# Kernel tuning notes

Measured on AMD Instinct MI355X. Metric: run time of the kernel, lower is better.

Reference implementation:

```python
import jax, jax.numpy as jnp
import numpy as np

T, B, NIN, NOUT, H, NLAYER = 512, 32, 72, 90, 512, 5


def _ln(x, g, b):
    m = jnp.mean(x, -1, keepdims=True)
    v = jnp.var(x, -1, keepdims=True)
    return (x - m) * jax.lax.rsqrt(v + 1e-5) * g + b


def _sru_dir(xt, fp, rp, hw, vf, vr, bf, br):
    # xt/fp/rp/hw: (T, B, H) in scan order; elementwise gated recurrence
    def step(c, inp):
        x_t, f_t, r_t, hw_t = inp
        f = jax.nn.sigmoid(f_t + vf * c + bf)
        r = jax.nn.sigmoid(r_t + vr * c + br)
        c2 = f * c + (1.0 - f) * x_t
        h = r * jnp.tanh(c2) + (1.0 - r) * hw_t
        return c2, h
    c0 = jnp.zeros_like(xt[0])
    cT, hs = jax.lax.scan(step, c0, (xt, fp, rp, hw))
    return hs, cT


def _sru_layer(x, W, v, b, g, be, k):
    # x: (T, B, d_in); W: (d_in, 2*k*H); v,b: (2 dirs, 2 gates, H)
    Tl, Bl = x.shape[0], x.shape[1]
    xn = _ln(x, g, be)
    U = (xn @ W).reshape(Tl, Bl, 2, k, H)
    outs, cs = [], []
    for d in range(2):
        Ud = U[:, :, d]
        if d == 1:
            Ud = jnp.flip(Ud, 0)
        # highway: extra projection when d_in != H (k=4), else raw input (k=3)
        hw = Ud[:, :, 3] if k == 4 else (jnp.flip(x, 0) if d == 1 else x)
        hs, cT = _sru_dir(Ud[:, :, 0], Ud[:, :, 1], Ud[:, :, 2], hw,
                          v[d, 0], v[d, 1], b[d, 0], b[d, 1])
        if d == 1:
            hs = jnp.flip(hs, 0)
        outs.append(hs)
        cs.append(cT)
    return jnp.concatenate(outs, -1), jnp.concatenate(cs, -1)


def setup_inputs() -> dict:
    key = jax.random.key(0)
    ks = jax.random.split(key, 12)
    s1 = 1.0 / np.sqrt(NIN)
    s2 = 1.0 / np.sqrt(2 * H)
    s0 = 1.0 / np.sqrt(H)
    return {
        "x": jax.random.normal(ks[0], (T, B, NIN), jnp.float32),
        "W1": jax.random.normal(ks[1], (NIN, H), jnp.float32) * s1,
        "b1": jnp.zeros((H,), jnp.float32),
        "W2": jax.random.normal(ks[2], (2 * H, NOUT), jnp.float32) * s2,
        "b2": jnp.zeros((NOUT,), jnp.float32),
        # SRU layer 0: input H -> 2 dirs * H, k=3 (highway uses raw input)
        "W0": jax.random.normal(ks[3], (H, 2 * 3 * H), jnp.float32) * s0,
        "v0": jax.random.normal(ks[4], (2, 2, H), jnp.float32) * s0,
        "bb0": jnp.zeros((2, 2, H), jnp.float32),
        "g0": jnp.ones((H,), jnp.float32),
        "be0": jnp.zeros((H,), jnp.float32),
        # SRU layers 1..4: input 2H -> 2 dirs * H, k=4 (projected highway)
        "Ws": jax.random.normal(ks[5], (NLAYER - 1, 2 * H, 2 * 4 * H), jnp.float32) * s2,
        "vs": jax.random.normal(ks[6], (NLAYER - 1, 2, 2, H), jnp.float32) * s0,
        "bbs": jnp.zeros((NLAYER - 1, 2, 2, H), jnp.float32),
        "gs": jnp.ones((NLAYER - 1, 2 * H), jnp.float32),
        "bes": jnp.zeros((NLAYER - 1, 2 * H), jnp.float32),
    }


def reference(x, W1, b1, W2, b2, W0, v0, bb0, g0, be0, Ws, vs, bbs, gs, bes):
    h = jax.nn.relu(x @ W1 + b1)  # (T, B, H); dropout is identity at eval
    states = []
    h, c = _sru_layer(h, W0, v0, bb0, g0, be0, 3)
    states.append(c)
    for i in range(Ws.shape[0]):
        h, c = _sru_layer(h, Ws[i], vs[i], bbs[i], gs[i], bes[i], 4)
        states.append(c)
    out = h @ W2 + b2  # (T, B, NOUT)
    return out, jnp.stack(states)  # h state: (NLAYER, B, 2H)
```

## Files before the change

kernel.cpp:

```cpp
#include <hip/hip_runtime.h>
#include <stdint.h>

#define T_LEN 512
#define BATCH 32
#define NIN   72
#define NOUT  90
#define HDIM  512
#define MROWS (T_LEN*BATCH)

typedef unsigned short u16;
typedef unsigned int   u32;

typedef __bf16 bf16x8 __attribute__((ext_vector_type(8)));
typedef short  s16x8  __attribute__((ext_vector_type(8)));
typedef float  f32x4  __attribute__((ext_vector_type(4)));

__device__ __forceinline__ float b2f(u16 u){ return __uint_as_float(((u32)u)<<16); }
__device__ __forceinline__ u16 f2b(float x){
  u32 u = __float_as_uint(x);
  u += 0x7FFFu + ((u>>16)&1u);
  return (u16)(u>>16);
}
__device__ __forceinline__ float sigmoidf_(float z){ return 1.f/(1.f+__expf(-z)); }
__device__ __forceinline__ float tanhf_(float z){ return 2.f/(1.f+__expf(-2.f*z)) - 1.f; }

__device__ __forceinline__ void gload16(const void* g, void* l){
  __builtin_amdgcn_global_load_lds(
      (const __attribute__((address_space(1))) void*)g,
      (__attribute__((address_space(3))) void*)l, 16, 0, 0);
}

__global__ __launch_bounds__(256) void k_transpose_cast(
    const float* __restrict__ S, u16* __restrict__ D, int K, int N, int ldd)
{
  __shared__ float t[32][33];
  int k0 = blockIdx.y*32, n0 = blockIdx.x*32;
  int tx = threadIdx.x, ty = threadIdx.y;
  #pragma unroll
  for (int i=0;i<4;++i){
    int k = k0 + ty + i*8, n = n0 + tx;
    if (k < K && n < N) t[ty+i*8][tx] = S[(size_t)k*N + n];
  }
  __syncthreads();
  #pragma unroll
  for (int i=0;i<4;++i){
    int n = n0 + ty + i*8, k = k0 + tx;
    if (n < N && k < K) D[(size_t)n*ldd + k] = f2b(t[tx][ty+i*8]);
  }
}

__global__ __launch_bounds__(256) void k_gemm1_relu(
    const float* __restrict__ X, const float* __restrict__ W1,
    const float* __restrict__ b1, u16* __restrict__ H0)
{
  __shared__ float As[64][73];
  __shared__ float Bs[72][64];
  int m0 = blockIdx.y*64, n0 = blockIdx.x*64;
  int tid = threadIdx.x;
  for (int idx=tid; idx<64*NIN; idx+=256){ int r=idx/NIN, k=idx-r*NIN; As[r][k] = X[(size_t)(m0+r)*NIN + k]; }
  for (int idx=tid; idx<NIN*64; idx+=256){ int k=idx>>6, n=idx&63; Bs[k][n] = W1[(size_t)k*HDIM + n0+n]; }
  __syncthreads();
  int tx = tid & 15, ty = tid >> 4;
  float acc[4][4] = {};
  for (int k=0;k<NIN;++k){
    float a[4], bv[4];
    #pragma unroll
    for (int i=0;i<4;++i) a[i]=As[ty*4+i][k];
    #pragma unroll
    for (int j=0;j<4;++j) bv[j]=Bs[k][tx*4+j];
    #pragma unroll
    for (int i=0;i<4;++i)
      #pragma unroll
      for (int j=0;j<4;++j) acc[i][j] += a[i]*bv[j];
  }
  #pragma unroll
  for (int i=0;i<4;++i){
    int row = m0 + ty*4 + i;
    #pragma unroll
    for (int j=0;j<4;++j){
      int col = n0 + tx*4 + j;
      float v = acc[i][j] + b1[col];
      H0[(size_t)row*HDIM + col] = f2b(v > 0.f ? v : 0.f);
    }
  }
}

template<int D>
__global__ __launch_bounds__(256) void k_ln(
    const u16* __restrict__ X, const float* __restrict__ g,
    const float* __restrict__ be, u16* __restrict__ Y)
{
  int wrow = (blockIdx.x*256 + threadIdx.x) >> 6;
  int lane = threadIdx.x & 63;
  constexpr int E = D/64;
  const u16* row = X + (size_t)wrow*D;
  float vals[E];
  float s=0.f, s2=0.f;
  #pragma unroll
  for (int i=0;i<E/4;++i){
    ushort4 u = *(const ushort4*)(row + i*256 + lane*4);
    float v0=b2f(u.x), v1=b2f(u.y), v2=b2f(u.z), v3=b2f(u.w);
    vals[i*4+0]=v0; vals[i*4+1]=v1; vals[i*4+2]=v2; vals[i*4+3]=v3;
    s  += v0+v1+v2+v3;
    s2 += v0*v0+v1*v1+v2*v2+v3*v3;
  }
  #pragma unroll
  for (int off=32; off; off>>=1){ s += __shfl_xor(s,off); s2 += __shfl_xor(s2,off); }
  float mean = s * (1.f/D);
  float var  = s2 * (1.f/D) - mean*mean;
  float rstd = rsqrtf(var + 1e-5f);
  u16* yr = Y + (size_t)wrow*D;
  #pragma unroll
  for (int i=0;i<E/4;++i){
    int col = i*256 + lane*4;
    float4 gg = *(const float4*)(g+col);
    float4 bb = *(const float4*)(be+col);
    ushort4 o;
    o.x = f2b((vals[i*4+0]-mean)*rstd*gg.x + bb.x);
    o.y = f2b((vals[i*4+1]-mean)*rstd*gg.y + bb.y);
    o.z = f2b((vals[i*4+2]-mean)*rstd*gg.z + bb.z);
    o.w = f2b((vals[i*4+3]-mean)*rstd*gg.w + bb.w);
    *(ushort4*)(yr + col) = o;
  }
}

__global__ __launch_bounds__(512, 2) void k_gemm256(
    const u16* __restrict__ A, const u16* __restrict__ BT,
    u16* __restrict__ C, int K, int N)
{
  __shared__ u16 lds[65536];
  const int tid  = threadIdx.x;
  const int lane = tid & 63;
  const int wid  = tid >> 6;
  const int wm   = wid >> 2;
  const int wn   = wid & 3;

  const int nbx = gridDim.x;
  const int nwg = nbx * gridDim.y;
  const int bid = blockIdx.y * nbx + blockIdx.x;
  const int cpx = nwg >> 3;
  const int swz = (bid & 7) * cpx + (bid >> 3);
  const int m0 = (swz / nbx) * 256;
  const int n0 = (swz % nbx) * 256;

  const int l3 = lane >> 3, l7 = lane & 7;
  const int kswz = (l7 ^ l3) * 8;

  auto stageA = [&](int ts, int h, int db){
    const u16* base = A + (size_t)(m0 + h*128 + wid*8 + l3)*K + ts*64 + kswz;
    u16* dst = lds + db*32768 + h*8192 + wid*512;
    gload16(base,               dst);
    gload16(base + (size_t)64*K, dst + 4096);
  };
  auto stageB = [&](int ts, int db){
    const u16* base = BT + (size_t)(n0 + wid*8 + l3)*K + ts*64 + kswz;
    u16* dst = lds + db*32768 + 16384 + wid*512;
    gload16(base,                dst);
    gload16(base + (size_t) 64*K, dst + 4096);
    gload16(base + (size_t)128*K, dst + 8192);
    gload16(base + (size_t)192*K, dst + 12288);
  };
  auto rdfrag = [&](const u16* buf, int row, int ks)->bf16x8 {
    int byte = (row*128 + (ks*32 + ((lane>>4)*8))*2) ^ ((row&7)<<4);
    return __builtin_bit_cast(bf16x8, *(const s16x8*)((const char*)buf + byte));
  };

  f32x4 acc[8][4] = {};
  const int nt = K >> 6;

  stageB(0, 0);
  stageA(0, 0, 0);
  stageA(0, 1, 0);

  for (int t = 0; t < nt; ++t){
    const u16* bufA = lds + (t & 1)*32768;
    const u16* bufB = bufA + 16384;
    const int tn = (t+1 < nt) ? t+1 : t;
    const int db = (t+1) & 1;

    stageB(tn, db);
    stageA(tn, 0, db);
    stageA(tn, 1, db);
    asm volatile("s_waitcnt vmcnt(8)" ::: "memory");
    __builtin_amdgcn_sched_barrier(0);
    __builtin_amdgcn_s_barrier();
    __builtin_amdgcn_sched_barrier(0);

    bf16x8 bfr[4][2];
    #pragma unroll
    for (int n=0;n<4;++n)
      #pragma unroll
      for (int ks=0;ks<2;++ks)
        bfr[n][ks] = rdfrag(bufB, wn*64 + n*16 + (lane&15), ks);
    bf16x8 afr[2][2][2];
    #pragma unroll
    for (int mm=0;mm<2;++mm)
      #pragma unroll
      for (int ks=0;ks<2;++ks)
        afr[0][mm][ks] = rdfrag(bufA, wm*128 + mm*16 + (lane&15), ks);

    #pragma unroll
    for (int q=0;q<4;++q){
      asm volatile("s_waitcnt lgkmcnt(0)" ::: "memory");
      __builtin_amdgcn_sched_barrier(0);
      __builtin_amdgcn_s_setprio(1);
      #pragma unroll
      for (int mm=0;mm<2;++mm)
        #pragma unroll
        for (int n=0;n<4;++n)
          #pragma unroll
          for (int ks=0;ks<2;++ks)
            acc[q*2+mm][n] = __builtin_amdgcn_mfma_f32_16x16x32_bf16(
                afr[q&1][mm][ks], bfr[n][ks], acc[q*2+mm][n], 0,0,0);
      __builtin_amdgcn_s_setprio(0);
      if (q < 3){
        #pragma unroll
        for (int mm=0;mm<2;++mm)
          #pragma unroll
          for (int ks=0;ks<2;++ks)
            afr[(q+1)&1][mm][ks] = rdfrag(bufA, wm*128 + ((q+1)*2+mm)*16 + (lane&15), ks);
      } else {
        asm volatile("s_waitcnt lgkmcnt(0)" ::: "memory");
      }
      __builtin_amdgcn_sched_barrier(0);
      __builtin_amdgcn_s_barrier();
      __builtin_amdgcn_sched_barrier(0);
    }
  }

  #pragma unroll
  for (int m=0;m<8;++m){
    int row = m0 + wm*128 + m*16 + ((lane>>4)<<2);
    #pragma unroll
    for (int n=0;n<4;++n){
      int col = n0 + wn*64 + n*16 + (lane&15);
      #pragma unroll
      for (int i=0;i<4;++i)
        C[(size_t)(row+i)*N + col] = f2b(acc[m][n][i]);
    }
  }
}

template<bool OUT_F32, bool HAS_BIAS>
__global__ __launch_bounds__(256) void k_gemm(
    const u16* __restrict__ A, const u16* __restrict__ BT,
    void* __restrict__ Cv, const float* __restrict__ bias,
    int K, int N, int ldc, int nbound)
{
  __shared__ u16 As[128*64];
  __shared__ u16 Bs[128*64];
  const int tid  = threadIdx.x;
  const int lane = tid & 63;
  const int wid  = tid >> 6;

  const int nbx = gridDim.x;
  const int nwg = nbx * gridDim.y;
  const int bid = blockIdx.y * nbx + blockIdx.x;
  const int cpx = nwg >> 3;
  const int swzb = (bid & 7) * cpx + (bid >> 3);
  const int bx = swzb % nbx, by = swzb / nbx;

  const int m0 = by * 128;
  const int n0 = bx * 128;
  const int wr = wid >> 1, wc = wid & 1;
  f32x4 acc[4][4] = {};

  const int srow = lane >> 3;
  const int skel = (lane & 7) * 8;

  for (int kt = 0; kt < K; kt += 64) {
    #pragma unroll
    for (int i=0;i<4;++i){
      int seg  = wid*4 + i;
      int arow = seg*8 + srow;
      gload16(A  + (size_t)(m0 + arow)*K + kt + skel, As + seg*512);
      gload16(BT + (size_t)(n0 + arow)*K + kt + skel, Bs + seg*512);
    }
    __syncthreads();
    #pragma unroll
    for (int ks=0; ks<2; ++ks){
      bf16x8 a[4], b[4];
      #pragma unroll
      for (int m=0;m<4;++m){
        int off = (wr*64 + m*16 + (lane&15))*64 + ks*32 + (lane>>4)*8;
        a[m] = __builtin_bit_cast(bf16x8, *(const s16x8*)(As + off));
      }
      #pragma unroll
      for (int n=0;n<4;++n){
        int off = (wc*64 + n*16 + (lane&15))*64 + ks*32 + (lane>>4)*8;
        b[n] = __builtin_bit_cast(bf16x8, *(const s16x8*)(Bs + off));
      }
      #pragma unroll
      for (int m=0;m<4;++m)
        #pragma unroll
        for (int n=0;n<4;++n)
          acc[m][n] = __builtin_amdgcn_mfma_f32_16x16x32_bf16(a[m], b[n], acc[m][n], 0,0,0);
    }
    __syncthreads();
  }

  #pragma unroll
  for (int m=0;m<4;++m){
    #pragma unroll
    for (int n=0;n<4;++n){
      int col = n0 + wc*64 + n*16 + (lane & 15);
      #pragma unroll
      for (int i=0;i<4;++i){
        int row = m0 + wr*64 + m*16 + ((lane>>4)<<2) + i;
        float v = acc[m][n][i];
        if (OUT_F32) {
          if (col < nbound){
            float bv = HAS_BIAS ? bias[col] : 0.f;
            ((float*)Cv)[(size_t)row*ldc + col] = v + bv;
          }
        } else {
          ((u16*)Cv)[(size_t)row*ldc + col] = f2b(v);
        }
      }
    }
  }
}

template<int KG>
__global__ __launch_bounds__(64) void k_scan(
    const u16* __restrict__ U, const u16* __restrict__ hwsrc,
    const float* __restrict__ v, const float* __restrict__ bb,
    u16* __restrict__ hout, float* __restrict__ states)
{
  constexpr int NS = 16;
  constexpr int D  = 14;
  constexpr int NITER = T_LEN/2;
  __shared__ u16 ring[NS*512];

  const int lane = threadIdx.x;
  const int bid  = blockIdx.x;
  const int hblk = bid & 7;
  const int b    = (bid >> 3) & 31;
  const int d    = bid >> 8;
  const int h    = hblk*64 + lane;
  const int RS   = 2*KG*HDIM;

  const int s2 = lane >> 5, p = (lane>>3)&3, c7 = lane&7;

  auto issue = [&](int k, int slot){
    int s = 2*k + s2;
    int t = d ? (T_LEN-1-s) : s;
    int row = t*BATCH + b;
    const u16* g;
    if (KG == 4 || p < 3)
      g = U + (size_t)row*RS + (size_t)(d*KG + p)*HDIM + hblk*64 + c7*8;
    else
      g = hwsrc + (size_t)row*HDIM + hblk*64 + c7*8;
    gload16(g, &ring[slot*512]);
  };

  for (int k=0;k<D;++k) issue(k, k);
  asm volatile("s_waitcnt vmcnt(0)" ::: "memory");
  __builtin_amdgcn_sched_barrier(0);

  const float vf  = v[(d*2+0)*HDIM + h];
  const float vr  = v[(d*2+1)*HDIM + h];
  const float bf_ = bb[(d*2+0)*HDIM + h];
  const float br_ = bb[(d*2+1)*HDIM + h];

  float cst = 0.f;
  for (int k=0;k<NITER;++k){
    int kk = (k+D < NITER) ? (k+D) : (NITER-1);
    issue(kk, (k+D) & (NS-1));
    asm volatile("s_waitcnt vmcnt(42)" ::: "memory");
    __builtin_amdgcn_sched_barrier(0);

    const int slot = k & (NS-1);
    #pragma unroll
    for (int j=0;j<2;++j){
      int s = 2*k + j;
      int t = d ? (T_LEN-1-s) : s;
      const u16* base = ring + slot*512 + j*256;
      float xv = b2f(base[0*64 + lane]);
      float fv = b2f(base[1*64 + lane]);
      float rv = b2f(base[2*64 + lane]);
      float wv = b2f(base[3*64 + lane]);
      float f = sigmoidf_(fv + vf*cst + bf_);
      float r = sigmoidf_(rv + vr*cst + br_);
      cst = f*cst + (1.f-f)*xv;
      float hv = r*tanhf_(cst) + (1.f-r)*wv;
      hout[(size_t)(t*BATCH + b)*(2*HDIM) + d*HDIM + h] = f2b(hv);
    }
  }
  states[(size_t)b*(2*HDIM) + d*HDIM + h] = cst;
}

extern "C" void kernel_launch(void* const* d_in, const int* in_sizes, int n_in,
                              void* d_out, int out_size, void* d_ws, size_t ws_size,
                              hipStream_t stream)
{
  const float* x   = (const float*)d_in[0];
  const float* W1  = (const float*)d_in[1];
  const float* b1  = (const float*)d_in[2];
  const float* W2  = (const float*)d_in[3];
  const float* b2  = (const float*)d_in[4];
  const float* W0  = (const float*)d_in[5];
  const float* v0  = (const float*)d_in[6];
  const float* bb0 = (const float*)d_in[7];
  const float* g0  = (const float*)d_in[8];
  const float* be0 = (const float*)d_in[9];
  const float* Ws  = (const float*)d_in[10];
  const float* vs  = (const float*)d_in[11];
  const float* bbs = (const float*)d_in[12];
  const float* gs  = (const float*)d_in[13];
  const float* bes = (const float*)d_in[14];
  (void)in_sizes; (void)n_in; (void)out_size; (void)ws_size;

  char* ws = (char*)d_ws;
  size_t off = 0;
  auto alloc = [&](size_t bytes)->void*{
    void* p = ws + off; off += (bytes + 255) & ~(size_t)255; return p;
  };
  u16* W0T  = (u16*)alloc((size_t)3072*512*2);
  u16* WsT  = (u16*)alloc((size_t)4*4096*1024*2);
  u16* W2T  = (u16*)alloc((size_t)128*1024*2);
  u16* h0   = (u16*)alloc((size_t)MROWS*512*2);
  u16* xn   = (u16*)alloc((size_t)MROWS*1024*2);
  u16* Ubuf = (u16*)alloc((size_t)MROWS*4096*2);
  u16* hbuf = (u16*)alloc((size_t)MROWS*1024*2);

  float* outp   = (float*)d_out;
  float* states = outp + (size_t)MROWS*NOUT;

  hipMemsetAsync(W2T, 0, (size_t)128*1024*2, stream);
  k_transpose_cast<<<dim3(3072/32, 512/32), dim3(32,8), 0, stream>>>(W0, W0T, 512, 3072, 512);
  for (int i=0;i<4;++i)
    k_transpose_cast<<<dim3(4096/32, 1024/32), dim3(32,8), 0, stream>>>(
        Ws + (size_t)i*1024*4096, WsT + (size_t)i*4096*1024, 1024, 4096, 1024);
  k_transpose_cast<<<dim3(3, 1024/32), dim3(32,8), 0, stream>>>(W2, W2T, 1024, NOUT, 1024);

  k_gemm1_relu<<<dim3(HDIM/64, MROWS/64), 256, 0, stream>>>(x, W1, b1, h0);

  k_ln<512><<<MROWS/4, 256, 0, stream>>>(h0, g0, be0, xn);
  k_gemm256<<<dim3(3072/256, MROWS/256), 512, 0, stream>>>(xn, W0T, Ubuf, 512, 3072);
  k_scan<3><<<512, 64, 0, stream>>>(Ubuf, h0, v0, bb0, hbuf, states);

  for (int i=0;i<4;++i){
    k_ln<1024><<<MROWS/4, 256, 0, stream>>>(hbuf, gs + (size_t)i*1024, bes + (size_t)i*1024, xn);
    k_gemm256<<<dim3(4096/256, MROWS/256), 512, 0, stream>>>(
        xn, WsT + (size_t)i*4096*1024, Ubuf, 1024, 4096);
    k_scan<4><<<512, 64, 0, stream>>>(Ubuf, nullptr, vs + (size_t)i*2048, bbs + (size_t)i*2048,
                                      hbuf, states + (size_t)(i+1)*BATCH*1024);
  }

  k_gemm<true,true><<<dim3(1, MROWS/128), 256, 0, stream>>>(
      hbuf, W2T, d_out, b2, 1024, 128, NOUT, NOUT);
}
```

Before: 1.262 ms.

## Software-pipeline GEMM LDS fragment loads and cut per-substep barriers

Restructures the bf16 MFMA GEMM main loop so each K-tile needs only one workgroup barrier instead of one per sub-step. The first fragment loads for the next tile are issued right after that barrier and overlap with the final MFMA group of the current tile, and the initial tile is loaded before the loop. The goal is to cut barrier stalls and LDS-read latency between MFMA groups. In exchange it waits for all outstanding global loads (vmcnt(0)) at the end of each tile, which can expose memory latency, and it raises register pressure by keeping fragments live across iterations.

```diff
diff --git a/kernel.cpp b/kernel.cpp
--- a/kernel.cpp
+++ b/kernel.cpp
@@ -166,41 +166,41 @@
   };
 
   f32x4 acc[8][4] = {};
+  bf16x8 bfr[4][2];
+  bf16x8 afr[2][2][2];
   const int nt = K >> 6;
 
   stageB(0, 0);
   stageA(0, 0, 0);
   stageA(0, 1, 0);
+  asm volatile("s_waitcnt vmcnt(0)" ::: "memory");
+  __builtin_amdgcn_sched_barrier(0);
+  __builtin_amdgcn_s_barrier();
+  __builtin_amdgcn_sched_barrier(0);
+  #pragma unroll
+  for (int n=0;n<4;++n)
+    #pragma unroll
+    for (int ks=0;ks<2;++ks)
+      bfr[n][ks] = rdfrag(lds + 16384, wn*64 + n*16 + (lane&15), ks);
+  #pragma unroll
+  for (int mm=0;mm<2;++mm)
+    #pragma unroll
+    for (int ks=0;ks<2;++ks)
+      afr[0][mm][ks] = rdfrag(lds, wm*128 + mm*16 + (lane&15), ks);
 
   for (int t = 0; t < nt; ++t){
-    const u16* bufA = lds + (t & 1)*32768;
-    const u16* bufB = bufA + 16384;
-    const int tn = (t+1 < nt) ? t+1 : t;
-    const int db = (t+1) & 1;
+    const u16* bufA  = lds + (t & 1)*32768;
+    const int  tn    = (t+1 < nt) ? t+1 : t;
+    const int  db    = (t+1) & 1;
+    const u16* bufAn = lds + db*32768;
+    const u16* bufBn = bufAn + 16384;
 
     stageB(tn, db);
     stageA(tn, 0, db);
     stageA(tn, 1, db);
-    asm volatile("s_waitcnt vmcnt(8)" ::: "memory");
-    __builtin_amdgcn_sched_barrier(0);
-    __builtin_amdgcn_s_barrier();
-    __builtin_amdgcn_sched_barrier(0);
-
-    bf16x8 bfr[4][2];
-    #pragma unroll
-    for (int n=0;n<4;++n)
-      #pragma unroll
-      for (int ks=0;ks<2;++ks)
-        bfr[n][ks] = rdfrag(bufB, wn*64 + n*16 + (lane&15), ks);
-    bf16x8 afr[2][2][2];
-    #pragma unroll
-    for (int mm=0;mm<2;++mm)
-      #pragma unroll
-      for (int ks=0;ks<2;++ks)
-        afr[0][mm][ks] = rdfrag(bufA, wm*128 + mm*16 + (lane&15), ks);
-
-    #pragma unroll
-    for (int q=0;q<4;++q){
+
+    #pragma unroll
+    for (int q=0;q<3;++q){
       asm volatile("s_waitcnt lgkmcnt(0)" ::: "memory");
       __builtin_amdgcn_sched_barrier(0);
       __builtin_amdgcn_s_setprio(1);
@@ -213,19 +213,37 @@
             acc[q*2+mm][n] = __builtin_amdgcn_mfma_f32_16x16x32_bf16(
                 afr[q&1][mm][ks], bfr[n][ks], acc[q*2+mm][n], 0,0,0);
       __builtin_amdgcn_s_setprio(0);
-      if (q < 3){
+      #pragma unroll
+      for (int mm=0;mm<2;++mm)
         #pragma unroll
-        for (int mm=0;mm<2;++mm)
-          #pragma unroll
-          for (int ks=0;ks<2;++ks)
-            afr[(q+1)&1][mm][ks] = rdfrag(bufA, wm*128 + ((q+1)*2+mm)*16 + (lane&15), ks);
-      } else {
-        asm volatile("s_waitcnt lgkmcnt(0)" ::: "memory");
-      }
-      __builtin_amdgcn_sched_barrier(0);
-      __builtin_amdgcn_s_barrier();
-      __builtin_amdgcn_sched_barrier(0);
-    }
+        for (int ks=0;ks<2;++ks)
+          afr[(q+1)&1][mm][ks] = rdfrag(bufA, wm*128 + ((q+1)*2+mm)*16 + (lane&15), ks);
+    }
+
+    asm volatile("s_waitcnt vmcnt(0) lgkmcnt(0)" ::: "memory");
+    __builtin_amdgcn_sched_barrier(0);
+    __builtin_amdgcn_s_barrier();
+    __builtin_amdgcn_sched_barrier(0);
+    #pragma unroll
+    for (int mm=0;mm<2;++mm)
+      #pragma unroll
+      for (int ks=0;ks<2;++ks)
+        afr[0][mm][ks] = rdfrag(bufAn, wm*128 + mm*16 + (lane&15), ks);
+    __builtin_amdgcn_s_setprio(1);
+    #pragma unroll
+    for (int mm=0;mm<2;++mm)
+      #pragma unroll
+      for (int n=0;n<4;++n)
+        #pragma unroll
+        for (int ks=0;ks<2;++ks)
+          acc[6+mm][n] = __builtin_amdgcn_mfma_f32_16x16x32_bf16(
+              afr[1][mm][ks], bfr[n][ks], acc[6+mm][n], 0,0,0);
+    __builtin_amdgcn_s_setprio(0);
+    #pragma unroll
+    for (int n=0;n<4;++n)
+      #pragma unroll
+      for (int ks=0;ks<2;++ks)
+        bfr[n][ks] = rdfrag(bufBn, wn*64 + n*16 + (lane&15), ks);
   }
 
   #pragma unroll
```

Result: no change. 1.274 ms (+1.0%).
